# Kernel optimization log

Measured on AMD Instinct MI355X. Metric: run time of the kernel, lower is better.

The kernel has to match this reference:

```python
import jax, jax.numpy as jnp
import numpy as np

N = 50000   # input points
E = 800000  # edges
M = 25000   # sampled points (ratio 0.5)
K = 15      # num_neighbors
H = 128     # hidden_dim
BN_EPS = 1e-5


def setup_inputs() -> dict:
    key = jax.random.key(0)
    ks = jax.random.split(key, 16)
    w = lambda k, s: jax.random.normal(k, s, dtype=jnp.float32) * 0.02
    z = lambda s: jnp.zeros(s, jnp.float32)
    o = lambda s: jnp.ones(s, jnp.float32)
    return {
        'points': jax.random.normal(ks[0], (N, 3), jnp.float32),
        'edge_index': jax.random.randint(ks[1], (2, E), 0, N),
        'sampled_idx': jnp.sort(jax.random.randint(ks[2], (M,), 0, N)),
        'neighbors': jax.random.randint(ks[3], (M, K), 0, M),
        'W1': w(ks[4], (3, H)), 'b1': z(H), 'g1': o(H), 'beta1': z(H),
        'W2': w(ks[5], (H, H)), 'b2': z(H), 'g2': o(H), 'beta2': z(H),
        'Wc': w(ks[6], (H, H)), 'bc': z(H),
        'Wn': w(ks[7], (H, H)), 'bn_b': z(H),
        'Wq': w(ks[8], (H, H // 2)), 'bq': z(H // 2),
        'Wk': w(ks[9], (H, H // 2)), 'bk': z(H // 2),
        'Wcat': w(ks[10], (H + 3, H + 3)), 'bcat': z(H + 3),
        'Wout': w(ks[11], (H + 3, 3)), 'bout': z(3),
    }


def _bn(x, g, b):
    # BatchNorm1d in training mode: batch mean, biased batch var
    m = x.mean(axis=0)
    v = x.var(axis=0)
    return g * (x - m) * jax.lax.rsqrt(v + BN_EPS) + b


def reference(points, edge_index, sampled_idx, neighbors,
              W1, b1, g1, beta1, W2, b2, g2, beta2,
              Wc, bc, Wn, bn_b, Wq, bq, Wk, bk, Wcat, bcat, Wout, bout):
    n = points.shape[0]
    # PointMLP x2: Linear -> BN -> ReLU
    x = jax.nn.relu(_bn(points @ W1 + b1, g1, beta1))
    x = jax.nn.relu(_bn(x @ W2 + b2, g2, beta2))
    # CustomGNN: relu(W_c x + mean_{j in N(i)} W_n x_j)
    src, dst = edge_index[0], edge_index[1]
    msg = (x @ Wn + bn_b)[src]                                   # [E, H]
    agg = jax.ops.segment_sum(msg, dst, num_segments=n)          # [N, H]
    cnt = jax.ops.segment_sum(jnp.ones(src.shape, jnp.float32), dst, num_segments=n)
    agg = agg / jnp.maximum(cnt, 1.0)[:, None]
    x = jax.nn.relu(x @ Wc + bc + agg)
    # sampling (indices precomputed, like fps output)
    sp = points[sampled_idx]                                     # [M, 3]
    sx = x[sampled_idx]                                          # [M, H]
    # AttentionLayer, fully vectorized over sampled points
    q = sx @ Wq + bq                                             # [M, H/2]
    nb_x = sx[neighbors]                                         # [M, K, H]
    k = nb_x @ Wk + bk                                           # [M, K, H/2]
    scale = jnp.sqrt(jnp.float32(q.shape[-1])) + 1e-6
    scores = jnp.einsum('md,mkd->mk', q, k) / scale              # [M, K]
    mask = (neighbors != 0).astype(jnp.float32)                  # quirk preserved
    attn = jax.nn.softmax(scores * mask, axis=1)                 # [M, K]
    rel = sp[neighbors] - sp[:, None, :]                         # [M, K, 3]
    cat = jnp.concatenate([nb_x, rel], axis=-1)                  # [M, K, H+3]
    proc = cat @ Wcat + bcat                                     # [M, K, H+3]
    aggf = jnp.einsum('mk,mkd->md', attn, proc)                  # [M, H+3]
    disp = aggf @ Wout + bout                                    # [M, 3]
    refined = sp + disp
    return refined, sx
```

## Files before the change

kernel.cpp:

```cpp
#include <hip/hip_runtime.h>
#include <climits>

#define NPTS 50000
#define NE   800000
#define MS   25000
#define KN   15
#define HD   128

__device__ __forceinline__ float wave_sum(float v) {
#pragma unroll
    for (int o = 32; o > 0; o >>= 1) v += __shfl_xor(v, o, 64);
    return v;
}

__launch_bounds__(256)
__global__ void prep_kernel(const float* __restrict__ Wq, const float* __restrict__ bq,
                            const float* __restrict__ Wk, const float* __restrict__ bk,
                            const float* __restrict__ Wcat, const float* __restrict__ bcat,
                            const float* __restrict__ Wout, const float* __restrict__ bout,
                            const float* __restrict__ Wc, const float* __restrict__ Wn,
                            float* __restrict__ Wqk, float* __restrict__ biasQK,
                            float* __restrict__ WcWn,
                            float* __restrict__ Wco128, float* __restrict__ w3, float* __restrict__ bco,
                            int* __restrict__ inv, int* __restrict__ cnt, int* __restrict__ cursor) {
    int b = blockIdx.x, tid = threadIdx.x;
    if (b < 64) {
        int i = b * 256 + tid;
        int k = i >> 7, c = i & 127;
        Wqk[i] = (c < 64) ? Wq[k * 64 + c] : Wk[k * 64 + (c - 64)];
    } else if (b < 192) {
        int i = (b - 64) * 256 + tid;
        int k = i >> 7, c = i & 127;
        WcWn[i] = (k < 128) ? Wc[k * 128 + c] : Wn[(k - 128) * 128 + c];
    } else if (b == 192) {
        if (tid < 128) biasQK[tid] = (tid < 64) ? bq[tid] : bk[tid - 64];
    } else if (b < 293) {
        int wid = tid >> 6, lane = tid & 63;
        int out = (b - 193) * 4 + wid;
        if (out < 396) {
            int r = out / 3, j = out - r * 3;
            const float* src = (r < 131) ? &Wcat[r * 131] : bcat;
            float s = 0.f;
            s = fmaf(src[lane], Wout[lane * 3 + j], s);
            s = fmaf(src[lane + 64], Wout[(lane + 64) * 3 + j], s);
            if (lane < 3) s = fmaf(src[lane + 128], Wout[(lane + 128) * 3 + j], s);
            s = wave_sum(s);
            if (lane == 0) {
                if (r < 128) Wco128[r * 3 + j] = s;
                else if (r < 131) w3[(r - 128) * 3 + j] = s;
                else bco[j] = s + bout[j];
            }
        }
    } else {
        int i = (b - 293) * 256 + tid;
        if (i < NPTS) inv[i] = INT_MAX;
        if (i < MS) { cnt[i] = 0; cursor[i] = 0; }
    }
}

__launch_bounds__(256)
__global__ void lin1_kernel(const float* __restrict__ pts, const float* __restrict__ W1,
                            const float* __restrict__ b1, float* __restrict__ y1,
                            float* __restrict__ psum, float* __restrict__ psq,
                            const int* __restrict__ smp, int* __restrict__ inv) {
    if (blockIdx.x >= 1000) {
        int m = (blockIdx.x - 1000) * 256 + threadIdx.x;
        if (m < MS) atomicMin(&inv[smp[m]], m);
        return;
    }
    int c = threadIdx.x & 127;
    int half = threadIdx.x >> 7;
    int part = blockIdx.x * 2 + half;
    float w0 = W1[c], w1 = W1[128 + c], w2 = W1[256 + c], bb = b1[c];
    float s = 0.f, s2 = 0.f;
    int r0 = part * 25, r1 = r0 + 25; if (r1 > NPTS) r1 = NPTS;
    for (int r = r0; r < r1; ++r) {
        float p0 = pts[r * 3], p1 = pts[r * 3 + 1], p2 = pts[r * 3 + 2];
        float y = fmaf(p0, w0, fmaf(p1, w1, fmaf(p2, w2, bb)));
        y1[r * HD + c] = y;
        s += y; s2 = fmaf(y, y, s2);
    }
    psum[part * 128 + c] = s;
    psq[part * 128 + c] = s2;
}

__launch_bounds__(256)
__global__ void bn_fin_par(const float* __restrict__ psum, const float* __restrict__ psq, int nb,
                           const float* __restrict__ g, const float* __restrict__ beta,
                           float* __restrict__ tp) {
    int c = blockIdx.x;
    int t = threadIdx.x;
    float S = 0.f, S2 = 0.f;
    for (int b = t; b < nb; b += 256) {
        S += psum[b * 128 + c];
        S2 += psq[b * 128 + c];
    }
    S = wave_sum(S); S2 = wave_sum(S2);
    __shared__ float sA[4], sB[4];
    int wid = t >> 6, lane = t & 63;
    if (lane == 0) { sA[wid] = S; sB[wid] = S2; }
    __syncthreads();
    if (t == 0) {
        float Sa = sA[0] + sA[1] + sA[2] + sA[3];
        float Sb = sB[0] + sB[1] + sB[2] + sB[3];
        const float invN = 1.f / (float)NPTS;
        float mean = Sa * invN;
        float var = Sb * invN - mean * mean;
        float a = g[c] * rsqrtf(var + 1e-5f);
        tp[c] = a;
        tp[128 + c] = beta[c] - mean * a;
    }
}

template <int R, bool TRANS, bool STATS, bool COUNT>
__launch_bounds__(256)
__global__ void gemm_bn(const float* __restrict__ A, int nrows, int gemmBlocks,
                        const float* __restrict__ W, const float* __restrict__ bias,
                        const float* __restrict__ tp,
                        float* __restrict__ Out,
                        float* __restrict__ psum, float* __restrict__ psq,
                        const int* __restrict__ ei, const int* __restrict__ inv,
                        int* __restrict__ cnt) {
    if (COUNT && (int)blockIdx.x >= gemmBlocks) {
        int e = ((int)blockIdx.x - gemmBlocks) * 256 + threadIdx.x;
        if (e < NE) {
            int mr = inv[ei[NE + e]];
            if (mr < MS) atomicAdd(&cnt[mr], 1);
        }
        return;
    }
    const int ROWS = 8 * R;
    __shared__ float As[8 * R][68];
    __shared__ float Ws[64][128];
    int tid = threadIdx.x;
    int r0 = blockIdx.x * ROWS;
    int tc = tid & 31, tr = tid >> 5;
    int trR = tr * R, c0 = tc << 2;
    float acc[R][4] = {};

    for (int k0 = 0; k0 < 128; k0 += 64) {
        if (k0) __syncthreads();
        for (int i = tid; i < ROWS * 16; i += 256) {
            int r = i >> 4, c4 = (i & 15) << 2;
            int gr = r0 + r;
            float4 v = make_float4(0.f, 0.f, 0.f, 0.f);
            if (gr < nrows) {
                v = *reinterpret_cast<const float4*>(&A[gr * HD + k0 + c4]);
                if (TRANS) {
                    int gc = k0 + c4;
                    v.x = fmaxf(fmaf(tp[gc],     v.x, tp[128 + gc]),     0.f);
                    v.y = fmaxf(fmaf(tp[gc + 1], v.y, tp[128 + gc + 1]), 0.f);
                    v.z = fmaxf(fmaf(tp[gc + 2], v.z, tp[128 + gc + 2]), 0.f);
                    v.w = fmaxf(fmaf(tp[gc + 3], v.w, tp[128 + gc + 3]), 0.f);
                }
            }
            *reinterpret_cast<float4*>(&As[r][c4]) = v;
        }
        for (int i = tid; i < 64 * 32; i += 256) {
            int k = i >> 5, c4 = (i & 31) << 2;
            *reinterpret_cast<float4*>(&Ws[k][c4]) =
                *reinterpret_cast<const float4*>(&W[(k0 + k) * 128 + c4]);
        }
        __syncthreads();
#pragma unroll 2
        for (int k = 0; k < 64; k += 4) {
            float4 a[R];
#pragma unroll
            for (int i = 0; i < R; ++i)
                a[i] = *reinterpret_cast<const float4*>(&As[trR + i][k]);
#pragma unroll
            for (int kk = 0; kk < 4; ++kk) {
                const float4 wv = *reinterpret_cast<const float4*>(&Ws[k + kk][c0]);
#pragma unroll
                for (int i = 0; i < R; ++i) {
                    float av = kk == 0 ? a[i].x : kk == 1 ? a[i].y : kk == 2 ? a[i].z : a[i].w;
                    acc[i][0] = fmaf(av, wv.x, acc[i][0]);
                    acc[i][1] = fmaf(av, wv.y, acc[i][1]);
                    acc[i][2] = fmaf(av, wv.z, acc[i][2]);
                    acc[i][3] = fmaf(av, wv.w, acc[i][3]);
                }
            }
        }
    }

    const float4 bv = *reinterpret_cast<const float4*>(&bias[c0]);
    float cs[4] = {}, cq[4] = {};
#pragma unroll
    for (int i = 0; i < R; ++i) {
        int gr = r0 + trR + i;
        float o0 = acc[i][0] + bv.x, o1 = acc[i][1] + bv.y;
        float o2 = acc[i][2] + bv.z, o3 = acc[i][3] + bv.w;
        if (gr < nrows) {
            *reinterpret_cast<float4*>(&Out[gr * HD + c0]) = make_float4(o0, o1, o2, o3);
            if (STATS) {
                cs[0] += o0; cs[1] += o1; cs[2] += o2; cs[3] += o3;
                cq[0] = fmaf(o0, o0, cq[0]); cq[1] = fmaf(o1, o1, cq[1]);
                cq[2] = fmaf(o2, o2, cq[2]); cq[3] = fmaf(o3, o3, cq[3]);
            }
        }
    }
    if (STATS) {
        float* red = &As[0][0];
        __syncthreads();
        *reinterpret_cast<float4*>(&red[tr * 128 + c0]) = make_float4(cs[0], cs[1], cs[2], cs[3]);
        __syncthreads();
        if (tid < 128) {
            float s = 0.f;
#pragma unroll
            for (int t = 0; t < 8; ++t) s += red[t * 128 + tid];
            psum[blockIdx.x * 128 + tid] = s;
        }
        __syncthreads();
        *reinterpret_cast<float4*>(&red[tr * 128 + c0]) = make_float4(cq[0], cq[1], cq[2], cq[3]);
        __syncthreads();
        if (tid < 128) {
            float s = 0.f;
#pragma unroll
            for (int t = 0; t < 8; ++t) s += red[t * 128 + tid];
            psq[blockIdx.x * 128 + tid] = s;
        }
    }
}

__launch_bounds__(1024)
__global__ void scan_kernel(const int* __restrict__ cnt, int* __restrict__ offs) {
    const int C = 25;
    __shared__ int buf[1024];
    int tid = threadIdx.x;
    int loc[C];
    int run = 0;
    int base = tid * C;
#pragma unroll
    for (int i = 0; i < C; ++i) {
        int idx = base + i;
        int v = (idx < MS) ? cnt[idx] : 0;
        loc[i] = run; run += v;
    }
    buf[tid] = run;
    __syncthreads();
    for (int off = 1; off < 1024; off <<= 1) {
        int t = (tid >= off) ? buf[tid - off] : 0;
        __syncthreads();
        buf[tid] += t;
        __syncthreads();
    }
    int excl = buf[tid] - run;
#pragma unroll
    for (int i = 0; i < C; ++i) {
        int idx = base + i;
        if (idx < MS) offs[idx] = excl + loc[i];
    }
    if (tid == 1023) offs[MS] = buf[tid];
}

__launch_bounds__(256)
__global__ void scatter_kernel(const int* __restrict__ ei, const int* __restrict__ inv,
                               const int* __restrict__ offs, int* __restrict__ cursor,
                               int* __restrict__ elist) {
    int e = blockIdx.x * 256 + threadIdx.x;
    if (e < NE) {
        int mr = inv[ei[NE + e]];
        if (mr < MS) {
            int pos = atomicAdd(&cursor[mr], 1);
            elist[offs[mr] + pos] = ei[e];
        }
    }
}

__launch_bounds__(256)
__global__ void agg_kernel(const int* __restrict__ smp, const int* __restrict__ inv,
                           const int* __restrict__ offs, const int* __restrict__ elist,
                           const float* __restrict__ y2, const float* __restrict__ tp2,
                           float* __restrict__ aggX, float* __restrict__ hasE) {
    int tid = threadIdx.x, wid = tid >> 6, lane = tid & 63;
    int m = blockIdx.x * 4 + wid;
    if (m >= MS) return;
    int d = smp[m];
    if (inv[d] != m) return;
    int half = lane >> 5, c0 = (lane & 31) << 2;
    const float4 ta = *reinterpret_cast<const float4*>(&tp2[c0]);
    const float4 tb = *reinterpret_cast<const float4*>(&tp2[128 + c0]);
    int e0 = offs[m], e1 = offs[m + 1];
    float4 s0 = {0,0,0,0}, s1 = {0,0,0,0}, s2 = {0,0,0,0}, s3 = {0,0,0,0};
    int e = e0;
    for (; e + 7 < e1; e += 8) {
        float4 v[4];
#pragma unroll
        for (int u = 0; u < 4; ++u)
            v[u] = *reinterpret_cast<const float4*>(&y2[elist[e + 2 * u + half] * HD + c0]);
        s0.x += fmaxf(fmaf(ta.x, v[0].x, tb.x), 0.f); s0.y += fmaxf(fmaf(ta.y, v[0].y, tb.y), 0.f);
        s0.z += fmaxf(fmaf(ta.z, v[0].z, tb.z), 0.f); s0.w += fmaxf(fmaf(ta.w, v[0].w, tb.w), 0.f);
        s1.x += fmaxf(fmaf(ta.x, v[1].x, tb.x), 0.f); s1.y += fmaxf(fmaf(ta.y, v[1].y, tb.y), 0.f);
        s1.z += fmaxf(fmaf(ta.z, v[1].z, tb.z), 0.f); s1.w += fmaxf(fmaf(ta.w, v[1].w, tb.w), 0.f);
        s2.x += fmaxf(fmaf(ta.x, v[2].x, tb.x), 0.f); s2.y += fmaxf(fmaf(ta.y, v[2].y, tb.y), 0.f);
        s2.z += fmaxf(fmaf(ta.z, v[2].z, tb.z), 0.f); s2.w += fmaxf(fmaf(ta.w, v[2].w, tb.w), 0.f);
        s3.x += fmaxf(fmaf(ta.x, v[3].x, tb.x), 0.f); s3.y += fmaxf(fmaf(ta.y, v[3].y, tb.y), 0.f);
        s3.z += fmaxf(fmaf(ta.z, v[3].z, tb.z), 0.f); s3.w += fmaxf(fmaf(ta.w, v[3].w, tb.w), 0.f);
    }
    for (; e + 1 < e1; e += 2) {
        const float4 v = *reinterpret_cast<const float4*>(&y2[elist[e + half] * HD + c0]);
        s0.x += fmaxf(fmaf(ta.x, v.x, tb.x), 0.f); s0.y += fmaxf(fmaf(ta.y, v.y, tb.y), 0.f);
        s0.z += fmaxf(fmaf(ta.z, v.z, tb.z), 0.f); s0.w += fmaxf(fmaf(ta.w, v.w, tb.w), 0.f);
    }
    if (e < e1 && half == 0) {
        const float4 v = *reinterpret_cast<const float4*>(&y2[elist[e] * HD + c0]);
        s1.x += fmaxf(fmaf(ta.x, v.x, tb.x), 0.f); s1.y += fmaxf(fmaf(ta.y, v.y, tb.y), 0.f);
        s1.z += fmaxf(fmaf(ta.z, v.z, tb.z), 0.f); s1.w += fmaxf(fmaf(ta.w, v.w, tb.w), 0.f);
    }
    float tx = (s0.x + s1.x) + (s2.x + s3.x);
    float ty = (s0.y + s1.y) + (s2.y + s3.y);
    float tz = (s0.z + s1.z) + (s2.z + s3.z);
    float tw = (s0.w + s1.w) + (s2.w + s3.w);
    tx += __shfl_xor(tx, 32, 64); ty += __shfl_xor(ty, 32, 64);
    tz += __shfl_xor(tz, 32, 64); tw += __shfl_xor(tw, 32, 64);
    float rs = 1.f / fmaxf((float)(e1 - e0), 1.f);
    if (half == 0)
        *reinterpret_cast<float4*>(&aggX[m * HD + c0]) = make_float4(tx * rs, ty * rs, tz * rs, tw * rs);
    if (lane == 0) hasE[m] = (e1 > e0) ? 1.f : 0.f;
}

__launch_bounds__(256)
__global__ void gemm_sx(const float* __restrict__ y2, const float* __restrict__ aggX,
                        const float* __restrict__ hasE,
                        const int* __restrict__ smp, const int* __restrict__ inv,
                        const float* __restrict__ WcWn,
                        const float* __restrict__ bc, const float* __restrict__ bn_b,
                        const float* __restrict__ tp2,
                        float* __restrict__ sx) {
    const int R = 3;
    __shared__ float As[24][68];
    __shared__ float Ws[64][128];
    int tid = threadIdx.x;
    int r0 = blockIdx.x * 24;
    int tc = tid & 31, tr = tid >> 5;
    int trR = tr * R, c0 = tc << 2;
    float acc[R][4] = {};

    for (int kk = 0; kk < 4; ++kk) {
        if (kk) __syncthreads();
        for (int i = tid; i < 24 * 16; i += 256) {
            int r = i >> 4, c4 = (i & 15) << 2;
            int gr = r0 + r;
            float4 v = make_float4(0.f, 0.f, 0.f, 0.f);
            if (gr < MS) {
                int d = smp[gr];
                if (kk < 2) {
                    int gc = (kk << 6) + c4;
                    v = *reinterpret_cast<const float4*>(&y2[d * HD + gc]);
                    v.x = fmaxf(fmaf(tp2[gc],     v.x, tp2[128 + gc]),     0.f);
                    v.y = fmaxf(fmaf(tp2[gc + 1], v.y, tp2[128 + gc + 1]), 0.f);
                    v.z = fmaxf(fmaf(tp2[gc + 2], v.z, tp2[128 + gc + 2]), 0.f);
                    v.w = fmaxf(fmaf(tp2[gc + 3], v.w, tp2[128 + gc + 3]), 0.f);
                } else {
                    v = *reinterpret_cast<const float4*>(&aggX[inv[d] * HD + ((kk - 2) << 6) + c4]);
                }
            }
            *reinterpret_cast<float4*>(&As[r][c4]) = v;
        }
        for (int i = tid; i < 64 * 32; i += 256) {
            int k = i >> 5, c4 = (i & 31) << 2;
            *reinterpret_cast<float4*>(&Ws[k][c4]) =
                *reinterpret_cast<const float4*>(&WcWn[((kk << 6) + k) * 128 + c4]);
        }
        __syncthreads();
#pragma unroll 2
        for (int k = 0; k < 64; k += 4) {
            float4 a[R];
#pragma unroll
            for (int i = 0; i < R; ++i)
                a[i] = *reinterpret_cast<const float4*>(&As[trR + i][k]);
#pragma unroll
            for (int kq = 0; kq < 4; ++kq) {
                const float4 wv = *reinterpret_cast<const float4*>(&Ws[k + kq][c0]);
#pragma unroll
                for (int i = 0; i < R; ++i) {
                    float av = kq == 0 ? a[i].x : kq == 1 ? a[i].y : kq == 2 ? a[i].z : a[i].w;
                    acc[i][0] = fmaf(av, wv.x, acc[i][0]);
                    acc[i][1] = fmaf(av, wv.y, acc[i][1]);
                    acc[i][2] = fmaf(av, wv.z, acc[i][2]);
                    acc[i][3] = fmaf(av, wv.w, acc[i][3]);
                }
            }
        }
    }

    const float4 bcv = *reinterpret_cast<const float4*>(&bc[c0]);
    const float4 bnv = *reinterpret_cast<const float4*>(&bn_b[c0]);
#pragma unroll
    for (int i = 0; i < R; ++i) {
        int gr = r0 + trR + i;
        if (gr < MS) {
            float f = hasE[inv[smp[gr]]];
            float o0 = fmaxf(acc[i][0] + bcv.x + f * bnv.x, 0.f);
            float o1 = fmaxf(acc[i][1] + bcv.y + f * bnv.y, 0.f);
            float o2 = fmaxf(acc[i][2] + bcv.z + f * bnv.z, 0.f);
            float o3 = fmaxf(acc[i][3] + bcv.w + f * bnv.w, 0.f);
            *reinterpret_cast<float4*>(&sx[gr * HD + c0]) = make_float4(o0, o1, o2, o3);
        }
    }
}

__launch_bounds__(256)
__global__ void p3_kernel(const float* __restrict__ sx, const float* __restrict__ Wco128,
                          const int* __restrict__ smp, const float* __restrict__ pts,
                          float* __restrict__ p3, float* __restrict__ sp) {
    int wid = threadIdx.x >> 6, lane = threadIdx.x & 63;
    int m = blockIdx.x * 4 + wid;
    if (m >= MS) return;
    int c0 = lane << 1;
    const float2 v = *reinterpret_cast<const float2*>(&sx[m * HD + c0]);
    float q0 = v.x * Wco128[c0 * 3]     + v.y * Wco128[(c0 + 1) * 3];
    float q1 = v.x * Wco128[c0 * 3 + 1] + v.y * Wco128[(c0 + 1) * 3 + 1];
    float q2 = v.x * Wco128[c0 * 3 + 2] + v.y * Wco128[(c0 + 1) * 3 + 2];
    q0 = wave_sum(q0); q1 = wave_sum(q1); q2 = wave_sum(q2);
    int d = smp[m];
    if (lane == 0) { p3[m * 3] = q0; p3[m * 3 + 1] = q1; p3[m * 3 + 2] = q2; }
    if (lane < 3) sp[m * 3 + lane] = pts[d * 3 + lane];
}

__launch_bounds__(256)
__global__ void attn_kernel(const float* __restrict__ qk, const int* __restrict__ nbr,
                            const float* __restrict__ p3, const float* __restrict__ sp,
                            const float* __restrict__ w3, const float* __restrict__ bco,
                            float* __restrict__ refined) {
    int wid = threadIdx.x >> 6, lane = threadIdx.x & 63;
    int m = blockIdx.x * 4 + wid;
    if (m >= MS) return;
    float ql = qk[m * HD + lane];
    int nbv[KN];
    float s[KN];
#pragma unroll
    for (int j = 0; j < KN; ++j) nbv[j] = nbr[m * KN + j];
#pragma unroll
    for (int j = 0; j < KN; ++j) {
        float t = ql * qk[nbv[j] * HD + 64 + lane];
        t = wave_sum(t);
        s[j] = (nbv[j] != 0) ? t * (1.f / 8.000001f) : 0.f;
    }
    float mx = s[0];
#pragma unroll
    for (int j = 1; j < KN; ++j) mx = fmaxf(mx, s[j]);
    float den = 0.f;
#pragma unroll
    for (int j = 0; j < KN; ++j) { s[j] = __expf(s[j] - mx); den += s[j]; }
    float invd = 1.f / den;
    float sp0 = sp[m * 3], sp1 = sp[m * 3 + 1], sp2 = sp[m * 3 + 2];
    float a0 = 0.f, a1 = 0.f, a2 = 0.f;
#pragma unroll
    for (int j = 0; j < KN; ++j) {
        int nb = nbv[j];
        float wgt = s[j] * invd;
        float r0 = sp[nb * 3] - sp0, r1 = sp[nb * 3 + 1] - sp1, r2 = sp[nb * 3 + 2] - sp2;
        float g0 = p3[nb * 3]     + r0 * w3[0] + r1 * w3[3] + r2 * w3[6];
        float g1 = p3[nb * 3 + 1] + r0 * w3[1] + r1 * w3[4] + r2 * w3[7];
        float g2 = p3[nb * 3 + 2] + r0 * w3[2] + r1 * w3[5] + r2 * w3[8];
        a0 = fmaf(wgt, g0, a0); a1 = fmaf(wgt, g1, a1); a2 = fmaf(wgt, g2, a2);
    }
    if (lane == 0) {
        refined[m * 3]     = sp0 + a0 + bco[0];
        refined[m * 3 + 1] = sp1 + a1 + bco[1];
        refined[m * 3 + 2] = sp2 + a2 + bco[2];
    }
}

extern "C" void kernel_launch(void* const* d_in, const int* in_sizes, int n_in,
                              void* d_out, int out_size, void* d_ws, size_t ws_size,
                              hipStream_t stream) {
    const float* pts   = (const float*)d_in[0];
    const int*   ei    = (const int*)d_in[1];
    const int*   smp   = (const int*)d_in[2];
    const int*   nbr   = (const int*)d_in[3];
    const float* W1    = (const float*)d_in[4];
    const float* b1    = (const float*)d_in[5];
    const float* g1    = (const float*)d_in[6];
    const float* beta1 = (const float*)d_in[7];
    const float* W2    = (const float*)d_in[8];
    const float* b2    = (const float*)d_in[9];
    const float* g2    = (const float*)d_in[10];
    const float* beta2 = (const float*)d_in[11];
    const float* Wc    = (const float*)d_in[12];
    const float* bc    = (const float*)d_in[13];
    const float* Wn    = (const float*)d_in[14];
    const float* bn_b  = (const float*)d_in[15];
    const float* Wq    = (const float*)d_in[16];
    const float* bq    = (const float*)d_in[17];
    const float* Wk    = (const float*)d_in[18];
    const float* bk    = (const float*)d_in[19];
    const float* Wcat  = (const float*)d_in[20];
    const float* bcat  = (const float*)d_in[21];
    const float* Wout  = (const float*)d_in[22];
    const float* bout  = (const float*)d_in[23];
    (void)in_sizes; (void)n_in; (void)out_size; (void)ws_size;

    float* w = (float*)d_ws;
    size_t o = 0;
    float* y1     = w + o; o += 6400000;
    float* y2     = w + o; o += 6400000;
    float* aggX   = w + o; o += 3200000;
    float* qkb    = w + o; o += 3200000;
    float* psum   = w + o; o += 262144;
    float* psq    = w + o; o += 262144;
    float* tp1    = w + o; o += 256;
    float* tp2    = w + o; o += 256;
    float* Wqk    = w + o; o += 16384;
    float* biasQK = w + o; o += 128;
    float* WcWn   = w + o; o += 32768;
    float* Wco128 = w + o; o += 384;
    float* w3     = w + o; o += 16;
    float* bco    = w + o; o += 16;
    float* p3     = w + o; o += 75008;
    float* sp     = w + o; o += 75008;
    float* hasE   = w + o; o += 25008;
    int* ip    = (int*)(w + o);
    int* inv   = ip;            ip += NPTS;
    int* cnt   = ip;            ip += MS;
    int* cursor= ip;            ip += MS;
    int* offs  = ip;            ip += MS + 4;
    int* elist = ip;

    float* refined = (float*)d_out;
    float* sx      = (float*)d_out + 75000;

    prep_kernel<<<489, 256, 0, stream>>>(Wq, bq, Wk, bk, Wcat, bcat, Wout, bout, Wc, Wn,
                                         Wqk, biasQK, WcWn, Wco128, w3, bco,
                                         inv, cnt, cursor);
    lin1_kernel<<<1098, 256, 0, stream>>>(pts, W1, b1, y1, psum, psq, smp, inv);
    bn_fin_par<<<128, 256, 0, stream>>>(psum, psq, 2000, g1, beta1, tp1);
    gemm_bn<6, true, true, true><<<1042 + 3125, 256, 0, stream>>>(
        y1, NPTS, 1042, W2, b2, tp1, y2, psum, psq, ei, inv, cnt);
    bn_fin_par<<<128, 256, 0, stream>>>(psum, psq, 1042, g2, beta2, tp2);
    scan_kernel<<<1, 1024, 0, stream>>>(cnt, offs);
    scatter_kernel<<<3125, 256, 0, stream>>>(ei, inv, offs, cursor, elist);
    agg_kernel<<<6250, 256, 0, stream>>>(smp, inv, offs, elist, y2, tp2, aggX, hasE);
    gemm_sx<<<1042, 256, 0, stream>>>(y2, aggX, hasE, smp, inv, WcWn, bc, bn_b, tp2, sx);
    p3_kernel<<<6250, 256, 0, stream>>>(sx, Wco128, smp, pts, p3, sp);
    gemm_bn<3, false, false, false><<<1042, 256, 0, stream>>>(
        sx, MS, 1042, Wqk, biasQK, nullptr, qkb, nullptr, nullptr, nullptr, nullptr, nullptr);
    attn_kernel<<<6250, 256, 0, stream>>>(qkb, nbr, p3, sp, w3, bco, refined);
}
```

Measured before the change: 326.6 us.

## Fuse sx GEMM with QK projection and p3/sp computation in one kernel

Merges gemm_sx, the separate QK projection GEMM and p3_kernel into a single kernel. The sx tile is kept in shared memory and reused for the Wqk GEMM and the 3-column Wco projection, so sx is not re-read from global memory and two launches go away. The cost is extra shared memory per block (an added 24x132 tile) and a longer kernel, which may lower occupancy.

```diff
diff --git a/kernel.cpp b/kernel.cpp
--- a/kernel.cpp
+++ b/kernel.cpp
@@ -320,16 +320,20 @@
 }
 
 __launch_bounds__(256)
-__global__ void gemm_sx(const float* __restrict__ y2, const float* __restrict__ aggX,
-                        const float* __restrict__ hasE,
-                        const int* __restrict__ smp, const int* __restrict__ inv,
-                        const float* __restrict__ WcWn,
-                        const float* __restrict__ bc, const float* __restrict__ bn_b,
-                        const float* __restrict__ tp2,
-                        float* __restrict__ sx) {
+__global__ void gemm_sx_fused(const float* __restrict__ y2, const float* __restrict__ aggX,
+                              const float* __restrict__ hasE,
+                              const int* __restrict__ smp, const int* __restrict__ inv,
+                              const float* __restrict__ WcWn,
+                              const float* __restrict__ bc, const float* __restrict__ bn_b,
+                              const float* __restrict__ tp2,
+                              const float* __restrict__ Wqk, const float* __restrict__ biasQK,
+                              const float* __restrict__ Wco128, const float* __restrict__ pts,
+                              float* __restrict__ sx, float* __restrict__ qkb,
+                              float* __restrict__ p3, float* __restrict__ sp) {
     const int R = 3;
     __shared__ float As[24][68];
     __shared__ float Ws[64][128];
+    __shared__ float sxs[24][132];
     int tid = threadIdx.x;
     int r0 = blockIdx.x * 24;
     int tc = tid & 31, tr = tid >> 5;
@@ -384,38 +388,87 @@
         }
     }
 
-    const float4 bcv = *reinterpret_cast<const float4*>(&bc[c0]);
-    const float4 bnv = *reinterpret_cast<const float4*>(&bn_b[c0]);
-#pragma unroll
-    for (int i = 0; i < R; ++i) {
-        int gr = r0 + trR + i;
-        if (gr < MS) {
-            float f = hasE[inv[smp[gr]]];
-            float o0 = fmaxf(acc[i][0] + bcv.x + f * bnv.x, 0.f);
-            float o1 = fmaxf(acc[i][1] + bcv.y + f * bnv.y, 0.f);
-            float o2 = fmaxf(acc[i][2] + bcv.z + f * bnv.z, 0.f);
-            float o3 = fmaxf(acc[i][3] + bcv.w + f * bnv.w, 0.f);
-            *reinterpret_cast<float4*>(&sx[gr * HD + c0]) = make_float4(o0, o1, o2, o3);
-        }
-    }
-}
-
-__launch_bounds__(256)
-__global__ void p3_kernel(const float* __restrict__ sx, const float* __restrict__ Wco128,
-                          const int* __restrict__ smp, const float* __restrict__ pts,
-                          float* __restrict__ p3, float* __restrict__ sp) {
-    int wid = threadIdx.x >> 6, lane = threadIdx.x & 63;
-    int m = blockIdx.x * 4 + wid;
-    if (m >= MS) return;
-    int c0 = lane << 1;
-    const float2 v = *reinterpret_cast<const float2*>(&sx[m * HD + c0]);
-    float q0 = v.x * Wco128[c0 * 3]     + v.y * Wco128[(c0 + 1) * 3];
-    float q1 = v.x * Wco128[c0 * 3 + 1] + v.y * Wco128[(c0 + 1) * 3 + 1];
-    float q2 = v.x * Wco128[c0 * 3 + 2] + v.y * Wco128[(c0 + 1) * 3 + 2];
-    q0 = wave_sum(q0); q1 = wave_sum(q1); q2 = wave_sum(q2);
-    int d = smp[m];
-    if (lane == 0) { p3[m * 3] = q0; p3[m * 3 + 1] = q1; p3[m * 3 + 2] = q2; }
-    if (lane < 3) sp[m * 3 + lane] = pts[d * 3 + lane];
+    {
+        const float4 bcv = *reinterpret_cast<const float4*>(&bc[c0]);
+        const float4 bnv = *reinterpret_cast<const float4*>(&bn_b[c0]);
+#pragma unroll
+        for (int i = 0; i < R; ++i) {
+            int gr = r0 + trR + i;
+            float4 ov = make_float4(0.f, 0.f, 0.f, 0.f);
+            if (gr < MS) {
+                float f = hasE[inv[smp[gr]]];
+                ov.x = fmaxf(acc[i][0] + bcv.x + f * bnv.x, 0.f);
+                ov.y = fmaxf(acc[i][1] + bcv.y + f * bnv.y, 0.f);
+                ov.z = fmaxf(acc[i][2] + bcv.z + f * bnv.z, 0.f);
+                ov.w = fmaxf(acc[i][3] + bcv.w + f * bnv.w, 0.f);
+                *reinterpret_cast<float4*>(&sx[gr * HD + c0]) = ov;
+            }
+            *reinterpret_cast<float4*>(&sxs[trR + i][c0]) = ov;
+        }
+    }
+    __syncthreads();
+
+    float qacc[R][4] = {};
+    for (int kk = 0; kk < 2; ++kk) {
+        if (kk) __syncthreads();
+        for (int i = tid; i < 64 * 32; i += 256) {
+            int k = i >> 5, c4 = (i & 31) << 2;
+            *reinterpret_cast<float4*>(&Ws[k][c4]) =
+                *reinterpret_cast<const float4*>(&Wqk[((kk << 6) + k) * 128 + c4]);
+        }
+        __syncthreads();
+        int kb = kk << 6;
+#pragma unroll 2
+        for (int k = 0; k < 64; k += 4) {
+            float4 a[R];
+#pragma unroll
+            for (int i = 0; i < R; ++i)
+                a[i] = *reinterpret_cast<const float4*>(&sxs[trR + i][kb + k]);
+#pragma unroll
+            for (int kq = 0; kq < 4; ++kq) {
+                const float4 wv = *reinterpret_cast<const float4*>(&Ws[k + kq][c0]);
+#pragma unroll
+                for (int i = 0; i < R; ++i) {
+                    float av = kq == 0 ? a[i].x : kq == 1 ? a[i].y : kq == 2 ? a[i].z : a[i].w;
+                    qacc[i][0] = fmaf(av, wv.x, qacc[i][0]);
+                    qacc[i][1] = fmaf(av, wv.y, qacc[i][1]);
+                    qacc[i][2] = fmaf(av, wv.z, qacc[i][2]);
+                    qacc[i][3] = fmaf(av, wv.w, qacc[i][3]);
+                }
+            }
+        }
+    }
+    {
+        const float4 bqv = *reinterpret_cast<const float4*>(&biasQK[c0]);
+#pragma unroll
+        for (int i = 0; i < R; ++i) {
+            int gr = r0 + trR + i;
+            if (gr < MS) {
+                *reinterpret_cast<float4*>(&qkb[gr * HD + c0]) = make_float4(
+                    qacc[i][0] + bqv.x, qacc[i][1] + bqv.y,
+                    qacc[i][2] + bqv.z, qacc[i][3] + bqv.w);
+            }
+        }
+    }
+
+    {
+        int wid = tid >> 6, lane = tid & 63;
+        int cc = lane << 1;
+        float wa0 = Wco128[cc * 3],     wa1 = Wco128[cc * 3 + 1],     wa2 = Wco128[cc * 3 + 2];
+        float wb0 = Wco128[(cc+1) * 3], wb1 = Wco128[(cc+1) * 3 + 1], wb2 = Wco128[(cc+1) * 3 + 2];
+#pragma unroll
+        for (int rr = wid * 6; rr < wid * 6 + 6; ++rr) {
+            int m = r0 + rr;
+            if (m >= MS) break;
+            float vx = sxs[rr][cc], vy = sxs[rr][cc + 1];
+            float q0 = fmaf(vx, wa0, vy * wb0);
+            float q1 = fmaf(vx, wa1, vy * wb1);
+            float q2 = fmaf(vx, wa2, vy * wb2);
+            q0 = wave_sum(q0); q1 = wave_sum(q1); q2 = wave_sum(q2);
+            if (lane == 0) { p3[m * 3] = q0; p3[m * 3 + 1] = q1; p3[m * 3 + 2] = q2; }
+            if (lane < 3) sp[m * 3 + lane] = pts[smp[m] * 3 + lane];
+        }
+    }
 }
 
 __launch_bounds__(256)
@@ -532,9 +585,7 @@
     scan_kernel<<<1, 1024, 0, stream>>>(cnt, offs);
     scatter_kernel<<<3125, 256, 0, stream>>>(ei, inv, offs, cursor, elist);
     agg_kernel<<<6250, 256, 0, stream>>>(smp, inv, offs, elist, y2, tp2, aggX, hasE);
-    gemm_sx<<<1042, 256, 0, stream>>>(y2, aggX, hasE, smp, inv, WcWn, bc, bn_b, tp2, sx);
-    p3_kernel<<<6250, 256, 0, stream>>>(sx, Wco128, smp, pts, p3, sp);
-    gemm_bn<3, false, false, false><<<1042, 256, 0, stream>>>(
-        sx, MS, 1042, Wqk, biasQK, nullptr, qkb, nullptr, nullptr, nullptr, nullptr, nullptr);
+    gemm_sx_fused<<<1042, 256, 0, stream>>>(y2, aggX, hasE, smp, inv, WcWn, bc, bn_b, tp2,
+                                            Wqk, biasQK, Wco128, pts, sx, qkb, p3, sp);
     attn_kernel<<<6250, 256, 0, stream>>>(qkb, nbr, p3, sp, w3, bco, refined);
 }
```

After: 321.6 us. Within noise of the previous version (-1.5%).
